# Kernel optimization log

Measured on AMD Instinct MI355X. Metric: run time of the kernel, lower is better.

The kernel has to match this reference:

```python
import jax, jax.numpy as jnp
import numpy as np

N_SRC0, N_FTRS, N_HID, N_CLS = 200000, 128, 1500, 64
E0, E1 = 1600000, 500000
RES0, RES1 = 50000, 10000


def sage_conv(x, src, tgt, res_size, W_root, W_neigh, b):
    # mean aggregation of neighbor (source) features onto the first res_size target nodes
    msg = x[src]                                              # [E, F] gather
    summed = jax.ops.segment_sum(msg, tgt, num_segments=res_size)   # [res, F]
    cnt = jax.ops.segment_sum(jnp.ones((src.shape[0],), x.dtype), tgt, num_segments=res_size)
    mean = summed / jnp.maximum(cnt, 1.0)[:, None]
    return x[:res_size] @ W_root + mean @ W_neigh + b


def setup_inputs() -> dict:
    key = jax.random.key(0)
    ks = jax.random.split(key, 12)
    x = jax.random.normal(ks[0], (N_SRC0, N_FTRS), dtype=jnp.float32)
    edge_src0 = jax.random.randint(ks[1], (E0,), 0, N_SRC0)
    edge_tgt0 = jax.random.randint(ks[2], (E0,), 0, RES0)
    edge_src1 = jax.random.randint(ks[3], (E1,), 0, RES0)
    edge_tgt1 = jax.random.randint(ks[4], (E1,), 0, RES1)
    s1 = 1.0 / np.sqrt(N_FTRS)
    s2 = 1.0 / np.sqrt(N_HID)
    W1_root = jax.random.uniform(ks[5], (N_FTRS, N_HID), jnp.float32, -s1, s1)
    W1_neigh = jax.random.uniform(ks[6], (N_FTRS, N_HID), jnp.float32, -s1, s1)
    b1 = jax.random.uniform(ks[7], (N_HID,), jnp.float32, -s1, s1)
    W2_root = jax.random.uniform(ks[8], (N_HID, N_CLS), jnp.float32, -s2, s2)
    W2_neigh = jax.random.uniform(ks[9], (N_HID, N_CLS), jnp.float32, -s2, s2)
    b2 = jax.random.uniform(ks[10], (N_CLS,), jnp.float32, -s2, s2)
    return {
        "x": x,
        "W1_root": W1_root, "W1_neigh": W1_neigh, "b1": b1,
        "W2_root": W2_root, "W2_neigh": W2_neigh, "b2": b2,
        "edge_src0": edge_src0, "edge_tgt0": edge_tgt0,
        "edge_src1": edge_src1, "edge_tgt1": edge_tgt1,
        "res0": RES0, "res1": RES1,
    }


def reference(x, W1_root, W1_neigh, b1, W2_root, W2_neigh, b2,
              edge_src0, edge_tgt0, edge_src1, edge_tgt1, res0, res1):
    h = sage_conv(x, edge_src0, edge_tgt0, res0, W1_root, W1_neigh, b1)  # [res0, H]
    h = jax.nn.relu(h)
    # dropout p=0.5 is identity in eval mode
    out = sage_conv(h, edge_src1, edge_tgt1, res1, W2_root, W2_neigh, b2)  # [res1, C]
    return jax.nn.log_softmax(out, axis=1)
```

## Files before the change

### kernel.cpp

```cpp
#include <hip/hip_runtime.h>
#include <hip/hip_bf16.h>
#include <cstdint>
#include <cstddef>

#define NSRC   200000
#define NF     128
#define NHID   1500
#define NHIDP  1536
#define NCLS   64
#define E0N    1600000
#define E1N    500000
#define RES0   50000
#define RES1   10000

#define CH     4096
#define NCH0   ((E0N + CH - 1) / CH)
#define NCH1   ((E1N + CH - 1) / CH)
#define NB0    ((RES0 + 255) / 256)
#define NB1    ((RES1 + 255) / 256)

#define PREP_BLOCKS  ((256 * NHIDP + 128 * NHIDP + NHIDP + 255) / 256)
#define COPYX_BLOCKS ((NSRC * NF) / (256 * 8))

typedef __bf16 bf16x8 __attribute__((ext_vector_type(8)));
typedef float  f32x4  __attribute__((ext_vector_type(4)));
typedef unsigned short u16x8 __attribute__((ext_vector_type(8)));
typedef unsigned int u32;
typedef unsigned long long u64;

__device__ __forceinline__ unsigned short f2bf(float f) {
    union { float f; unsigned u; } v; v.f = f;
    unsigned r = v.u + 0x7fffu + ((v.u >> 16) & 1u);
    return (unsigned short)(r >> 16);
}
__device__ __forceinline__ float bf2f(unsigned short b) {
    union { u32 u; float f; } v; v.u = ((u32)b) << 16;
    return v.f;
}

__device__ __forceinline__ void lds_dma16(const void* g, void* lds) {
    __builtin_amdgcn_global_load_lds(
        (const __attribute__((address_space(1))) unsigned int*)g,
        (__attribute__((address_space(3))) unsigned int*)lds, 16, 0, 0);
}

__device__ __forceinline__ void raw_barrier() {
    __asm__ volatile("s_barrier" ::: "memory");
}
__device__ __forceinline__ void wait_vm4() {
    __asm__ volatile("s_waitcnt vmcnt(4)" ::: "memory");
}
__device__ __forceinline__ void wait_vm0() {
    __asm__ volatile("s_waitcnt vmcnt(0)" ::: "memory");
}
__device__ __forceinline__ void wait_lgkm0() {
    __asm__ volatile("s_waitcnt lgkmcnt(0)" ::: "memory");
}

__global__ __launch_bounds__(256) void setup_kernel(
        const float* __restrict__ x, unsigned short* __restrict__ xbf,
        const float* __restrict__ W1r, const float* __restrict__ W1n,
        const float* __restrict__ b1,
        const float* __restrict__ W2r, const float* __restrict__ W2n,
        unsigned short* __restrict__ WcatT, unsigned short* __restrict__ W2catT,
        float* __restrict__ b1e) {
    int bid = blockIdx.x;
    if (bid < PREP_BLOCKS) {
        int id = bid * 256 + threadIdx.x;
        if (id < 256 * NHIDP) {
            int n = id >> 8, k = id & 255;
            float v = 0.f;
            if (n < NHID) v = (k < NF) ? W1r[k * NHID + n] : W1n[(k - NF) * NHID + n];
            WcatT[n * 256 + k] = f2bf(v);
        } else {
            int id2 = id - 256 * NHIDP;
            if (id2 < 128 * NHIDP) {
                int n = id2 / NHIDP, k = id2 % NHIDP;
                float v = 0.f;
                if (k < NHID) v = (n < 64) ? W2n[k * 64 + n] : W2r[k * 64 + (n - 64)];
                W2catT[n * NHIDP + k] = f2bf(v);
            } else {
                int c = id2 - 128 * NHIDP;
                if (c < NHIDP) b1e[c] = (c < NHID) ? b1[c] : 0.f;
            }
        }
    } else {
        size_t i = ((size_t)(bid - PREP_BLOCKS) * 256 + threadIdx.x) * 8;
        const float4* s = (const float4*)(x + i);
        float4 a = s[0], b = s[1];
        u16x8 o;
        o[0] = f2bf(a.x); o[1] = f2bf(a.y); o[2] = f2bf(a.z); o[3] = f2bf(a.w);
        o[4] = f2bf(b.x); o[5] = f2bf(b.y); o[6] = f2bf(b.z); o[7] = f2bf(b.w);
        *(u16x8*)(xbf + i) = o;
    }
}

__device__ __forceinline__ void p1a_body(const int* __restrict__ tgt, int n,
                                         int nb, u32* __restrict__ H, int c) {
    __shared__ u32 lhist[256];
    int tid = threadIdx.x;
    lhist[tid] = 0;
    __syncthreads();
#pragma unroll
    for (int it = 0; it < CH / 256; ++it) {
        int i = c * CH + it * 256 + tid;
        if (i < n) atomicAdd(&lhist[((u32)tgt[i]) >> 8], 1u);
    }
    __syncthreads();
    if (tid < nb) H[c * nb + tid] = lhist[tid];
}

__global__ __launch_bounds__(256) void p1a_both_kernel(
        const int* __restrict__ t0, const int* __restrict__ t1,
        u32* __restrict__ H1, u32* __restrict__ H2) {
    int b = blockIdx.x;
    if (b < NCH0) p1a_body(t0, E0N, NB0, H1, b);
    else          p1a_body(t1, E1N, NB1, H2, b - NCH0);
}

__device__ __forceinline__ void bscan_body(const u32* __restrict__ H,
                                           int nch, int nb, int b,
                                           u32* __restrict__ base_rel,
                                           u32* __restrict__ Bsum) {
    __shared__ u32 part[512];
    int t = threadIdx.x;
    part[t] = (t < nch) ? H[t * nb + b] : 0u;
    __syncthreads();
    for (int d = 1; d < 512; d <<= 1) {
        u32 v = part[t];
        u32 add = (t >= d) ? part[t - d] : 0u;
        __syncthreads();
        part[t] = v + add;
        __syncthreads();
    }
    if (t < nch) base_rel[t * nb + b] = (t == 0) ? 0u : part[t - 1];
    if (t == 0) Bsum[b] = part[nch - 1];
}

__global__ __launch_bounds__(512) void bscan_both_kernel(
        const u32* __restrict__ H1, u32* __restrict__ base1, u32* __restrict__ Bsum1,
        const u32* __restrict__ H2, u32* __restrict__ base2, u32* __restrict__ Bsum2) {
    int b = blockIdx.x;
    if (b < NB0) bscan_body(H1, NCH0, NB0, b, base1, Bsum1);
    else         bscan_body(H2, NCH1, NB1, b - NB0, base2, Bsum2);
}

__global__ __launch_bounds__(256) void boff_kernel(const u32* __restrict__ Bsum1,
                                                   u32* __restrict__ boff1, int nb1,
                                                   const u32* __restrict__ Bsum2,
                                                   u32* __restrict__ boff2, int nb2) {
    const u32* B = blockIdx.x ? Bsum2 : Bsum1;
    u32* O = blockIdx.x ? boff2 : boff1;
    int nb = blockIdx.x ? nb2 : nb1;
    __shared__ u32 part[256];
    int t = threadIdx.x;
    part[t] = (t < nb) ? B[t] : 0u;
    __syncthreads();
    for (int d = 1; d < 256; d <<= 1) {
        u32 v = part[t];
        u32 add = (t >= d) ? part[t - d] : 0u;
        __syncthreads();
        part[t] = v + add;
        __syncthreads();
    }
    if (t < nb) O[t] = (t == 0) ? 0u : part[t - 1];
}

__device__ __forceinline__ void p1b_body(const int* __restrict__ src,
                                         const int* __restrict__ tgt, int n,
                                         int nb, const u32* __restrict__ base_rel,
                                         const u32* __restrict__ boff,
                                         u64* __restrict__ bucketed, int c) {
    __shared__ u32 lcur[256];
    __shared__ u32 lbase[256];
    int tid = threadIdx.x;
    lcur[tid] = 0;
    if (tid < nb) lbase[tid] = base_rel[c * nb + tid] + boff[tid];
    __syncthreads();
#pragma unroll
    for (int it = 0; it < CH / 256; ++it) {
        int i = c * CH + it * 256 + tid;
        if (i < n) {
            u32 t = (u32)tgt[i];
            u32 s = (u32)src[i];
            u32 b = t >> 8;
            u32 r = atomicAdd(&lcur[b], 1u);
            bucketed[lbase[b] + r] = ((u64)t << 32) | (u64)s;
        }
    }
}

__global__ __launch_bounds__(256) void p1b_both_kernel(
        const int* __restrict__ s0, const int* __restrict__ t0,
        const u32* __restrict__ base1, const u32* __restrict__ boff1,
        u64* __restrict__ bkt1,
        const int* __restrict__ s1, const int* __restrict__ t1,
        const u32* __restrict__ base2, const u32* __restrict__ boff2,
        u64* __restrict__ bkt2) {
    int b = blockIdx.x;
    if (b < NCH0) p1b_body(s0, t0, E0N, NB0, base1, boff1, bkt1, b);
    else          p1b_body(s1, t1, E1N, NB1, base2, boff2, bkt2, b - NCH0);
}

__device__ __forceinline__ void p2_body(const u64* __restrict__ bucketed,
                                        const u32* __restrict__ boff,
                                        int nb, int res, int etot,
                                        int* __restrict__ csr,
                                        u32* __restrict__ off_out,
                                        u32* __restrict__ cnt_out, int b) {
    __shared__ u32 lhist[256];
    __shared__ u32 part[256];
    __shared__ u32 cur[256];
    int tid = threadIdx.x;
    u32 start = boff[b];
    u32 end = (b == nb - 1) ? (u32)etot : boff[b + 1];
    u32 count = end - start;
    if (tid < 256) lhist[tid] = 0;
    __syncthreads();
    for (u32 i = tid; i < count; i += 1024) {
        u32 t = (u32)(bucketed[start + i] >> 32);
        atomicAdd(&lhist[t & 255u], 1u);
    }
    __syncthreads();
    if (tid < 256) part[tid] = lhist[tid];
    __syncthreads();
    for (int d = 1; d < 256; d <<= 1) {
        u32 v = (tid < 256) ? part[tid] : 0u;
        u32 add = (tid >= d && tid < 256) ? part[tid - d] : 0u;
        __syncthreads();
        if (tid < 256) part[tid] = v + add;
        __syncthreads();
    }
    if (tid < 256) {
        u32 excl = (tid == 0) ? 0u : part[tid - 1];
        cur[tid] = excl;
        int tg = (b << 8) + tid;
        if (tg < res) {
            off_out[tg] = start + excl;
            cnt_out[tg] = lhist[tid];
        }
    }
    __syncthreads();
    for (u32 i = tid; i < count; i += 1024) {
        u64 pr = bucketed[start + i];
        u32 lt = ((u32)(pr >> 32)) & 255u;
        u32 r = atomicAdd(&cur[lt], 1u);
        csr[start + r] = (int)(u32)pr;
    }
}

__global__ __launch_bounds__(1024) void p2_both_kernel(
        const u64* __restrict__ bkt1, const u32* __restrict__ boff1,
        int* __restrict__ csr1, u32* __restrict__ off1, u32* __restrict__ cnt1,
        const u64* __restrict__ bkt2, const u32* __restrict__ boff2,
        int* __restrict__ csr2, u32* __restrict__ off2, u32* __restrict__ cnt2) {
    int b = blockIdx.x;
    if (b < NB0) p2_body(bkt1, boff1, NB0, RES0, E0N, csr1, off1, cnt1, b);
    else         p2_body(bkt2, boff2, NB1, RES1, E1N, csr2, off2, cnt2, b - NB0);
}

__global__ __launch_bounds__(256) void agg1_csr_kernel(
        const unsigned short* __restrict__ xbf, const int* __restrict__ csr,
        const u32* __restrict__ off, const u32* __restrict__ cnt,
        unsigned short* __restrict__ mean1) {
    int row = blockIdx.x * 4 + (threadIdx.x >> 6);
    int lane = threadIdx.x & 63;
    if (row >= RES0) return;
    int q = lane >> 4, c16 = lane & 15;
    u32 base = off[row], deg = cnt[row];
    float acc[8] = {};
    u32 e = 0;
    for (; e + 8 <= deg; e += 8) {
        int s0 = csr[base + e + q];
        int s1 = csr[base + e + 4 + q];
        u16x8 v0 = *(const u16x8*)(xbf + (size_t)s0 * NF + c16 * 8);
        u16x8 v1 = *(const u16x8*)(xbf + (size_t)s1 * NF + c16 * 8);
#pragma unroll
        for (int i = 0; i < 8; ++i) acc[i] += bf2f(v0[i]) + bf2f(v1[i]);
    }
    for (; e + 4 <= deg; e += 4) {
        int s0 = csr[base + e + q];
        u16x8 v0 = *(const u16x8*)(xbf + (size_t)s0 * NF + c16 * 8);
#pragma unroll
        for (int i = 0; i < 8; ++i) acc[i] += bf2f(v0[i]);
    }
    if (e < deg) {
        bool valid = (e + q) < deg;
        int s0 = csr[base + (valid ? e + q : e)];
        u16x8 v0 = *(const u16x8*)(xbf + (size_t)s0 * NF + c16 * 8);
        if (valid) {
#pragma unroll
            for (int i = 0; i < 8; ++i) acc[i] += bf2f(v0[i]);
        }
    }
#pragma unroll
    for (int i = 0; i < 8; ++i) {
        acc[i] += __shfl_xor(acc[i], 32, 64);
        acc[i] += __shfl_xor(acc[i], 16, 64);
    }
    if (q == 0) {
        float inv = 1.0f / fmaxf((float)deg, 1.0f);
        u16x8 o;
#pragma unroll
        for (int i = 0; i < 8; ++i) o[i] = f2bf(acc[i] * inv);
        *(u16x8*)(mean1 + (size_t)row * NF + c16 * 8) = o;
    }
}

__device__ __forceinline__ void stage_chunk(
        const unsigned short* __restrict__ xbf, const unsigned short* __restrict__ mean1,
        const unsigned short* __restrict__ WcatT, int m0, int j, int kt,
        unsigned short* As, unsigned short* Bs, int wid, int lane) {
    int ksel = kt * 32;
    const unsigned short* srcA = (ksel < 128)
        ? xbf + (size_t)m0 * NF + ksel
        : mean1 + (size_t)m0 * NF + (ksel - 128);
#pragma unroll
    for (int ci = 0; ci < 2; ++ci) {
        int cb = ci * 256 + wid * 64;
        int chunk = cb + lane;
        int n = chunk >> 2, kc = chunk & 3;
        lds_dma16(srcA + (size_t)n * NF + kc * 8, &As[cb * 8]);
    }
    const unsigned short* srcB = WcatT + (size_t)(j * 128) * 256 + ksel;
#pragma unroll
    for (int ci = 0; ci < 2; ++ci) {
        int cb = ci * 256 + wid * 64;
        int chunk = cb + lane;
        int n = chunk >> 2, kc = chunk & 3;
        lds_dma16(srcB + (size_t)n * 256 + kc * 8, &Bs[cb * 8]);
    }
}

__global__ __launch_bounds__(256, 2) void fused_gemm_kernel(
        const unsigned short* __restrict__ xbf, const unsigned short* __restrict__ mean1,
        const unsigned short* __restrict__ WcatT, const float* __restrict__ b1e,
        const unsigned short* __restrict__ W2catT,
        float* __restrict__ pp0, float* __restrict__ pp1) {
    __shared__ __align__(16) unsigned short As[3][128 * 32];
    __shared__ __align__(16) unsigned short Bs[3][128 * 32];
    __shared__ __align__(16) unsigned short Ht[128 * 128];

    int m0 = blockIdx.x * 128;
    int jb = blockIdx.y * 6;
    float* pout = blockIdx.y ? pp1 : pp0;
    int tid = threadIdx.x;
    int lane = tid & 63, wid = tid >> 6;
    int wm = wid >> 1, wn = wid & 1;
    int quad = lane >> 4, l15 = lane & 15;

    f32x4 pacc[4][4] = {};

    stage_chunk(xbf, mean1, WcatT, m0, jb, 0, As[0], Bs[0], wid, lane);
    stage_chunk(xbf, mean1, WcatT, m0, jb, 1, As[1], Bs[1], wid, lane);

#pragma unroll
    for (int jj = 0; jj < 6; ++jj) {
        int j = jb + jj;
        f32x4 hacc[4][4] = {};
#pragma unroll
        for (int kt = 0; kt < 8; ++kt) {
            const int g = jj * 8 + kt;
            if (g == 47) wait_vm0(); else wait_vm4();
            raw_barrier();
            if (g + 2 < 48) {
                int g2 = g + 2;
                stage_chunk(xbf, mean1, WcatT, m0, jb + (g2 >> 3), g2 & 7,
                            As[g2 % 3], Bs[g2 % 3], wid, lane);
            }
            const unsigned short* Asb = As[g % 3];
            const unsigned short* Bsb = Bs[g % 3];
            bf16x8 a[4], b[4];
#pragma unroll
            for (int mi = 0; mi < 4; ++mi)
                a[mi] = *(const bf16x8*)(&Asb[(wm * 64 + mi * 16 + l15) * 32 + quad * 8]);
#pragma unroll
            for (int ni = 0; ni < 4; ++ni)
                b[ni] = *(const bf16x8*)(&Bsb[(wn * 64 + ni * 16 + l15) * 32 + quad * 8]);
#pragma unroll
            for (int mi = 0; mi < 4; ++mi)
#pragma unroll
                for (int ni = 0; ni < 4; ++ni)
                    hacc[mi][ni] = __builtin_amdgcn_mfma_f32_16x16x32_bf16(b[ni], a[mi], hacc[mi][ni], 0, 0, 0);
        }
#pragma unroll
        for (int ni = 0; ni < 4; ++ni) {
            int n0 = wn * 64 + ni * 16 + quad * 4;
            float4 bv = *(const float4*)(b1e + j * 128 + n0);
#pragma unroll
            for (int mi = 0; mi < 4; ++mi) {
                int m = wm * 64 + mi * 16 + l15;
                int gsw = ((n0 >> 3) ^ (m & 15));
                ushort4 o;
                o.x = f2bf(fmaxf(hacc[mi][ni][0] + bv.x, 0.f));
                o.y = f2bf(fmaxf(hacc[mi][ni][1] + bv.y, 0.f));
                o.z = f2bf(fmaxf(hacc[mi][ni][2] + bv.z, 0.f));
                o.w = f2bf(fmaxf(hacc[mi][ni][3] + bv.w, 0.f));
                *(ushort4*)(&Ht[m * 128 + gsw * 8 + (n0 & 7)]) = o;
            }
        }
        wait_lgkm0();
        raw_barrier();
#pragma unroll
        for (int kk2 = 0; kk2 < 128; kk2 += 32) {
            bf16x8 a2[4], b2[4];
#pragma unroll
            for (int mi = 0; mi < 4; ++mi) {
                int m = wm * 64 + mi * 16 + l15;
                int gr = (kk2 >> 3) + quad;
                int gsw = gr ^ (m & 15);
                a2[mi] = *(const bf16x8*)(&Ht[m * 128 + gsw * 8]);
            }
#pragma unroll
            for (int ni = 0; ni < 4; ++ni)
                b2[ni] = *(const bf16x8*)(W2catT + (size_t)(wn * 64 + ni * 16 + l15) * NHIDP
                                          + j * 128 + kk2 + quad * 8);
#pragma unroll
            for (int mi = 0; mi < 4; ++mi)
#pragma unroll
                for (int ni = 0; ni < 4; ++ni)
                    pacc[mi][ni] = __builtin_amdgcn_mfma_f32_16x16x32_bf16(b2[ni], a2[mi], pacc[mi][ni], 0, 0, 0);
        }
    }

#pragma unroll
    for (int mi = 0; mi < 4; ++mi) {
        int gr = m0 + wm * 64 + mi * 16 + l15;
        if (gr < RES0) {
#pragma unroll
            for (int ni = 0; ni < 4; ++ni) {
                int gc0 = wn * 64 + ni * 16 + quad * 4;
                *(float4*)(&pout[(size_t)gr * 128 + gc0]) = *(float4*)(&pacc[mi][ni]);
            }
        }
    }
}

__global__ __launch_bounds__(256) void padd_kernel(
        const float* __restrict__ pp0, const float* __restrict__ pp1,
        unsigned short* __restrict__ pnbf, float* __restrict__ root64) {
    int i = blockIdx.x * 256 + threadIdx.x;
    if (i >= RES0 * 8) return;
    int row = i >> 3, c8 = i & 7;
    size_t b = (size_t)row * 128 + c8 * 8;
    f32x4 s0 = *(const f32x4*)(pp0 + b)     + *(const f32x4*)(pp1 + b);
    f32x4 s1 = *(const f32x4*)(pp0 + b + 4) + *(const f32x4*)(pp1 + b + 4);
    u16x8 o;
    o[0] = f2bf(s0[0]); o[1] = f2bf(s0[1]); o[2] = f2bf(s0[2]); o[3] = f2bf(s0[3]);
    o[4] = f2bf(s1[0]); o[5] = f2bf(s1[1]); o[6] = f2bf(s1[2]); o[7] = f2bf(s1[3]);
    *(u16x8*)(pnbf + (size_t)row * 64 + c8 * 8) = o;
    if (row < RES1) {
        size_t rb = (size_t)row * 128 + 64 + c8 * 8;
        f32x4 r0 = *(const f32x4*)(pp0 + rb)     + *(const f32x4*)(pp1 + rb);
        f32x4 r1 = *(const f32x4*)(pp0 + rb + 4) + *(const f32x4*)(pp1 + rb + 4);
        *(f32x4*)(root64 + (size_t)row * 64 + c8 * 8)     = r0;
        *(f32x4*)(root64 + (size_t)row * 64 + c8 * 8 + 4) = r1;
    }
}

__global__ __launch_bounds__(256) void final_csr_kernel(
        const unsigned short* __restrict__ pnbf, const float* __restrict__ root64,
        const int* __restrict__ csr, const u32* __restrict__ off,
        const u32* __restrict__ cnt, const float* __restrict__ b2,
        float* __restrict__ out) {
    int row = blockIdx.x * 4 + (threadIdx.x >> 6);
    int lane = threadIdx.x & 63;
    if (row >= RES1) return;
    int es = lane >> 3, c8 = lane & 7;
    u32 base = off[row], deg = cnt[row];
    float acc[8] = {};
    u32 e = 0;
    for (; e + 8 <= deg; e += 8) {
        int s = csr[base + e + es];
        u16x8 v = *(const u16x8*)(pnbf + (size_t)s * 64 + c8 * 8);
#pragma unroll
        for (int i = 0; i < 8; ++i) acc[i] += bf2f(v[i]);
    }
    if (e < deg) {
        bool valid = (e + es) < deg;
        int s = csr[base + (valid ? e + es : e)];
        u16x8 v = *(const u16x8*)(pnbf + (size_t)s * 64 + c8 * 8);
        if (valid) {
#pragma unroll
            for (int i = 0; i < 8; ++i) acc[i] += bf2f(v[i]);
        }
    }
#pragma unroll
    for (int i = 0; i < 8; ++i) {
        acc[i] += __shfl_xor(acc[i], 32, 64);
        acc[i] += __shfl_xor(acc[i], 16, 64);
        acc[i] += __shfl_xor(acc[i], 8, 64);
    }
    float inv = 1.0f / fmaxf((float)deg, 1.0f);
    float v[8];
    const float* rp = root64 + (size_t)row * 64 + c8 * 8;
#pragma unroll
    for (int i = 0; i < 8; ++i) v[i] = rp[i] + acc[i] * inv + b2[c8 * 8 + i];
    float m = v[0];
#pragma unroll
    for (int i = 1; i < 8; ++i) m = fmaxf(m, v[i]);
    m = fmaxf(m, __shfl_xor(m, 1, 64));
    m = fmaxf(m, __shfl_xor(m, 2, 64));
    m = fmaxf(m, __shfl_xor(m, 4, 64));
    float s = 0.f;
#pragma unroll
    for (int i = 0; i < 8; ++i) s += expf(v[i] - m);
    s += __shfl_xor(s, 1, 64);
    s += __shfl_xor(s, 2, 64);
    s += __shfl_xor(s, 4, 64);
    if (es == 0) {
        float lg = logf(s);
        f32x4 o0, o1;
#pragma unroll
        for (int i = 0; i < 4; ++i) { o0[i] = v[i] - m - lg; o1[i] = v[i + 4] - m - lg; }
        *(f32x4*)(&out[(size_t)row * 64 + c8 * 8])     = o0;
        *(f32x4*)(&out[(size_t)row * 64 + c8 * 8 + 4]) = o1;
    }
}

extern "C" void kernel_launch(void* const* d_in, const int* in_sizes, int n_in,
                              void* d_out, int out_size, void* d_ws, size_t ws_size,
                              hipStream_t stream) {
    const float* x   = (const float*)d_in[0];
    const float* W1r = (const float*)d_in[1];
    const float* W1n = (const float*)d_in[2];
    const float* b1  = (const float*)d_in[3];
    const float* W2r = (const float*)d_in[4];
    const float* W2n = (const float*)d_in[5];
    const float* b2  = (const float*)d_in[6];
    const int* es0 = (const int*)d_in[7];
    const int* et0 = (const int*)d_in[8];
    const int* es1 = (const int*)d_in[9];
    const int* et1 = (const int*)d_in[10];
    float* out = (float*)d_out;

    char* ws = (char*)d_ws;
    const size_t PPBYTES = (size_t)RES0 * 128 * 4;
    float* pp1 = (float*)ws;
    size_t o0 = 0;
    auto alloc0 = [&](size_t bytes) {
        void* ptr = ws + o0;
        o0 = (o0 + bytes + 255) & ~(size_t)255;
        return ptr;
    };
    u64* bkt1  = (u64*)alloc0((size_t)E0N * 8);
    u64* bkt2  = (u64*)alloc0((size_t)E1N * 8);
    int* csr1  = (int*)alloc0((size_t)E0N * 4);
    u32* H1    = (u32*)alloc0((size_t)NCH0 * NB0 * 4);
    u32* base1 = (u32*)alloc0((size_t)NCH0 * NB0 * 4);
    u32* H2    = (u32*)alloc0((size_t)NCH1 * NB1 * 4);
    u32* base2 = (u32*)alloc0((size_t)NCH1 * NB1 * 4);
    u32* Bsum1 = (u32*)alloc0((size_t)NB0 * 4);
    u32* Bsum2 = (u32*)alloc0((size_t)NB1 * 4);
    u32* boff1 = (u32*)alloc0((size_t)NB0 * 4);
    u32* boff2 = (u32*)alloc0((size_t)NB1 * 4);
    u32* off1  = (u32*)alloc0((size_t)RES0 * 4);
    u32* cnt1  = (u32*)alloc0((size_t)RES0 * 4);

    size_t off_ = PPBYTES;
    auto alloc = [&](size_t bytes) {
        void* ptr = ws + off_;
        off_ = (off_ + bytes + 255) & ~(size_t)255;
        return ptr;
    };
    int* csr2  = (int*)alloc((size_t)E1N * 4);
    u32* off2  = (u32*)alloc((size_t)RES1 * 4);
    u32* cnt2  = (u32*)alloc((size_t)RES1 * 4);
    unsigned short* xbf    = (unsigned short*)alloc((size_t)NSRC * NF * 2);
    unsigned short* mean1  = (unsigned short*)alloc((size_t)(RES0 + 128) * NF * 2);
    unsigned short* WcatT  = (unsigned short*)alloc((size_t)NHIDP * 256 * 2);
    unsigned short* W2catT = (unsigned short*)alloc((size_t)128 * NHIDP * 2);
    float*          b1e    = (float*)alloc((size_t)NHIDP * 4);
    float*          pp0    = (float*)alloc(PPBYTES);
    unsigned short* pnbf   = (unsigned short*)alloc((size_t)RES0 * 64 * 2);
    float*          root64 = (float*)alloc((size_t)RES1 * 64 * 4);

    setup_kernel<<<PREP_BLOCKS + COPYX_BLOCKS, 256, 0, stream>>>(
        x, xbf, W1r, W1n, b1, W2r, W2n, WcatT, W2catT, b1e);

    p1a_both_kernel<<<NCH0 + NCH1, 256, 0, stream>>>(et0, et1, H1, H2);
    bscan_both_kernel<<<NB0 + NB1, 512, 0, stream>>>(H1, base1, Bsum1, H2, base2, Bsum2);
    boff_kernel<<<2, 256, 0, stream>>>(Bsum1, boff1, NB0, Bsum2, boff2, NB1);
    p1b_both_kernel<<<NCH0 + NCH1, 256, 0, stream>>>(
        es0, et0, base1, boff1, bkt1, es1, et1, base2, boff2, bkt2);
    p2_both_kernel<<<NB0 + NB1, 1024, 0, stream>>>(
        bkt1, boff1, csr1, off1, cnt1, bkt2, boff2, csr2, off2, cnt2);

    agg1_csr_kernel<<<(RES0 + 3) / 4, 256, 0, stream>>>(
        xbf, csr1, off1, cnt1, mean1);

    fused_gemm_kernel<<<dim3((RES0 + 127) / 128, 2), 256, 0, stream>>>(
        xbf, mean1, WcatT, b1e, W2catT, pp0, pp1);

    padd_kernel<<<(RES0 * 8 + 255) / 256, 256, 0, stream>>>(pp0, pp1, pnbf, root64);

    final_csr_kernel<<<(RES1 + 3) / 4, 256, 0, stream>>>(
        pnbf, root64, csr2, off2, cnt2, b2, out);
}
```

Measured before the change: 444.2 us.

## Shrink fused GEMM tile to 64 rows and keep hidden activations in registers

```diff
diff --git a/kernel.cpp b/kernel.cpp
--- a/kernel.cpp
+++ b/kernel.cpp
@@ -38,6 +38,12 @@
     return v.f;
 }
 
+__device__ __forceinline__ u32 cvt_pk_bf16(float lo, float hi) {
+    u32 r;
+    asm("v_cvt_pk_bf16_f32 %0, %1, %2" : "=v"(r) : "v"(lo), "v"(hi));
+    return r;
+}
+
 __device__ __forceinline__ void lds_dma16(const void* g, void* lds) {
     __builtin_amdgcn_global_load_lds(
         (const __attribute__((address_space(1))) unsigned int*)g,
@@ -47,14 +53,11 @@
 __device__ __forceinline__ void raw_barrier() {
     __asm__ volatile("s_barrier" ::: "memory");
 }
-__device__ __forceinline__ void wait_vm4() {
-    __asm__ volatile("s_waitcnt vmcnt(4)" ::: "memory");
+__device__ __forceinline__ void wait_vm3() {
+    __asm__ volatile("s_waitcnt vmcnt(3)" ::: "memory");
 }
 __device__ __forceinline__ void wait_vm0() {
     __asm__ volatile("s_waitcnt vmcnt(0)" ::: "memory");
-}
-__device__ __forceinline__ void wait_lgkm0() {
-    __asm__ volatile("s_waitcnt lgkmcnt(0)" ::: "memory");
 }
 
 __global__ __launch_bounds__(256) void setup_kernel(
@@ -307,41 +310,14 @@
     }
 }
 
-__device__ __forceinline__ void stage_chunk(
-        const unsigned short* __restrict__ xbf, const unsigned short* __restrict__ mean1,
-        const unsigned short* __restrict__ WcatT, int m0, int j, int kt,
-        unsigned short* As, unsigned short* Bs, int wid, int lane) {
-    int ksel = kt * 32;
-    const unsigned short* srcA = (ksel < 128)
-        ? xbf + (size_t)m0 * NF + ksel
-        : mean1 + (size_t)m0 * NF + (ksel - 128);
-#pragma unroll
-    for (int ci = 0; ci < 2; ++ci) {
-        int cb = ci * 256 + wid * 64;
-        int chunk = cb + lane;
-        int n = chunk >> 2, kc = chunk & 3;
-        lds_dma16(srcA + (size_t)n * NF + kc * 8, &As[cb * 8]);
-    }
-    const unsigned short* srcB = WcatT + (size_t)(j * 128) * 256 + ksel;
-#pragma unroll
-    for (int ci = 0; ci < 2; ++ci) {
-        int cb = ci * 256 + wid * 64;
-        int chunk = cb + lane;
-        int n = chunk >> 2, kc = chunk & 3;
-        lds_dma16(srcB + (size_t)n * 256 + kc * 8, &Bs[cb * 8]);
-    }
-}
-
-__global__ __launch_bounds__(256, 2) void fused_gemm_kernel(
+__global__ __launch_bounds__(256, 3) void fused_gemm_kernel(
         const unsigned short* __restrict__ xbf, const unsigned short* __restrict__ mean1,
         const unsigned short* __restrict__ WcatT, const float* __restrict__ b1e,
         const unsigned short* __restrict__ W2catT,
         float* __restrict__ pp0, float* __restrict__ pp1) {
-    __shared__ __align__(16) unsigned short As[3][128 * 32];
-    __shared__ __align__(16) unsigned short Bs[3][128 * 32];
-    __shared__ __align__(16) unsigned short Ht[128 * 128];
-
-    int m0 = blockIdx.x * 128;
+    __shared__ __align__(16) unsigned short buf[3][6144];
+
+    int m0 = blockIdx.x * 64;
     int jb = blockIdx.y * 6;
     float* pout = blockIdx.y ? pp1 : pp0;
     int tid = threadIdx.x;
@@ -349,90 +325,117 @@
     int wm = wid >> 1, wn = wid & 1;
     int quad = lane >> 4, l15 = lane & 15;
 
-    f32x4 pacc[4][4] = {};
-
-    stage_chunk(xbf, mean1, WcatT, m0, jb, 0, As[0], Bs[0], wid, lane);
-    stage_chunk(xbf, mean1, WcatT, m0, jb, 1, As[1], Bs[1], wid, lane);
+    const int rA = lane >> 2, kcs = (lane & 3) * 8;
+    const size_t offA = (size_t)rA * NF + kcs;
+    const size_t offB = (size_t)rA * 256 + kcs;
+    const unsigned short* Ax = xbf + (size_t)m0 * NF;
+    const unsigned short* Am = mean1 + (size_t)m0 * NF;
+
+    auto stage = [&](int g) {
+        int ksel = (g & 7) * 32;
+        const unsigned short* Asrc = (ksel < 128) ? (Ax + ksel) : (Am + (ksel - 128));
+        const unsigned short* Bsrc = WcatT + ((size_t)(jb + (g >> 3)) * 128) * 256 + ksel;
+        unsigned short* dst = &buf[g % 3][0];
+#pragma unroll
+        for (int i = 0; i < 3; ++i) {
+            int id = wid * 3 + i;
+            if (id < 4) lds_dma16(Asrc + (size_t)id * (16 * NF) + offA, dst + id * 512);
+            else        lds_dma16(Bsrc + (size_t)(id - 4) * (16 * 256) + offB, dst + id * 512);
+        }
+    };
+
+    f32x4 pacc[2][8] = {};
+
+    stage(0);
+    stage(1);
 
 #pragma unroll
     for (int jj = 0; jj < 6; ++jj) {
-        int j = jb + jj;
-        f32x4 hacc[4][4] = {};
+        const int j = jb + jj;
+        f32x4 hacc[2][4] = {};
 #pragma unroll
         for (int kt = 0; kt < 8; ++kt) {
             const int g = jj * 8 + kt;
-            if (g == 47) wait_vm0(); else wait_vm4();
+            if (g == 47) wait_vm0(); else wait_vm3();
             raw_barrier();
-            if (g + 2 < 48) {
-                int g2 = g + 2;
-                stage_chunk(xbf, mean1, WcatT, m0, jb + (g2 >> 3), g2 & 7,
-                            As[g2 % 3], Bs[g2 % 3], wid, lane);
-            }
-            const unsigned short* Asb = As[g % 3];
-            const unsigned short* Bsb = Bs[g % 3];
-            bf16x8 a[4], b[4];
-#pragma unroll
-            for (int mi = 0; mi < 4; ++mi)
-                a[mi] = *(const bf16x8*)(&Asb[(wm * 64 + mi * 16 + l15) * 32 + quad * 8]);
+            if (g + 2 < 48) stage(g + 2);
+            const unsigned short* Ab = &buf[g % 3][0];
+            const unsigned short* Bb = Ab + 2048;
+            bf16x8 a[2], b[4];
+#pragma unroll
+            for (int mi = 0; mi < 2; ++mi)
+                a[mi] = *(const bf16x8*)(Ab + (wm * 32 + mi * 16 + l15) * 32 + quad * 8);
 #pragma unroll
             for (int ni = 0; ni < 4; ++ni)
-                b[ni] = *(const bf16x8*)(&Bsb[(wn * 64 + ni * 16 + l15) * 32 + quad * 8]);
-#pragma unroll
-            for (int mi = 0; mi < 4; ++mi)
+                b[ni] = *(const bf16x8*)(Bb + (wn * 64 + ni * 16 + l15) * 32 + quad * 8);
+            __builtin_amdgcn_s_setprio(1);
+#pragma unroll
+            for (int mi = 0; mi < 2; ++mi)
 #pragma unroll
                 for (int ni = 0; ni < 4; ++ni)
                     hacc[mi][ni] = __builtin_amdgcn_mfma_f32_16x16x32_bf16(b[ni], a[mi], hacc[mi][ni], 0, 0, 0);
-        }
-#pragma unroll
-        for (int ni = 0; ni < 4; ++ni) {
-            int n0 = wn * 64 + ni * 16 + quad * 4;
-            float4 bv = *(const float4*)(b1e + j * 128 + n0);
-#pragma unroll
-            for (int mi = 0; mi < 4; ++mi) {
-                int m = wm * 64 + mi * 16 + l15;
-                int gsw = ((n0 >> 3) ^ (m & 15));
-                ushort4 o;
-                o.x = f2bf(fmaxf(hacc[mi][ni][0] + bv.x, 0.f));
-                o.y = f2bf(fmaxf(hacc[mi][ni][1] + bv.y, 0.f));
-                o.z = f2bf(fmaxf(hacc[mi][ni][2] + bv.z, 0.f));
-                o.w = f2bf(fmaxf(hacc[mi][ni][3] + bv.w, 0.f));
-                *(ushort4*)(&Ht[m * 128 + gsw * 8 + (n0 & 7)]) = o;
+            __builtin_amdgcn_s_setprio(0);
+        }
+
+        u32 a2w[2][2][4];
+#pragma unroll
+        for (int mi = 0; mi < 2; ++mi)
+#pragma unroll
+            for (int ni = 0; ni < 4; ++ni) {
+                float4 bv = *(const float4*)(b1e + j * 128 + wn * 64 + ni * 16 + quad * 4);
+                f32x4 h = hacc[mi][ni];
+                float h0 = fmaxf(h[0] + bv.x, 0.f);
+                float h1 = fmaxf(h[1] + bv.y, 0.f);
+                float h2 = fmaxf(h[2] + bv.z, 0.f);
+                float h3 = fmaxf(h[3] + bv.w, 0.f);
+                a2w[mi][ni >> 1][(ni & 1) * 2 + 0] = cvt_pk_bf16(h0, h1);
+                a2w[mi][ni >> 1][(ni & 1) * 2 + 1] = cvt_pk_bf16(h2, h3);
             }
-        }
-        wait_lgkm0();
-        raw_barrier();
-#pragma unroll
-        for (int kk2 = 0; kk2 < 128; kk2 += 32) {
-            bf16x8 a2[4], b2[4];
-#pragma unroll
-            for (int mi = 0; mi < 4; ++mi) {
-                int m = wm * 64 + mi * 16 + l15;
-                int gr = (kk2 >> 3) + quad;
-                int gsw = gr ^ (m & 15);
-                a2[mi] = *(const bf16x8*)(&Ht[m * 128 + gsw * 8]);
+        const unsigned short* W2p = W2catT + (size_t)(j * 128 + wn * 64 + quad * 4);
+        __builtin_amdgcn_s_setprio(1);
+#pragma unroll
+        for (int kk = 0; kk < 2; ++kk) {
+            union U { u32 w[4]; bf16x8 v; };
+            U A2[2];
+#pragma unroll
+            for (int mi = 0; mi < 2; ++mi)
+#pragma unroll
+                for (int w = 0; w < 4; ++w) A2[mi].w[w] = a2w[mi][kk][w];
+#pragma unroll
+            for (int ni2 = 0; ni2 < 8; ++ni2) {
+                size_t bb = (size_t)(ni2 * 16 + l15) * NHIDP + kk * 32;
+                uint2 lo = *(const uint2*)(W2p + bb);
+                uint2 hi = *(const uint2*)(W2p + bb + 16);
+                U B2; B2.w[0] = lo.x; B2.w[1] = lo.y; B2.w[2] = hi.x; B2.w[3] = hi.y;
+#pragma unroll
+                for (int mi = 0; mi < 2; ++mi)
+                    pacc[mi][ni2] = __builtin_amdgcn_mfma_f32_16x16x32_bf16(B2.v, A2[mi].v, pacc[mi][ni2], 0, 0, 0);
             }
-#pragma unroll
-            for (int ni = 0; ni < 4; ++ni)
-                b2[ni] = *(const bf16x8*)(W2catT + (size_t)(wn * 64 + ni * 16 + l15) * NHIDP
-                                          + j * 128 + kk2 + quad * 8);
-#pragma unroll
-            for (int mi = 0; mi < 4; ++mi)
-#pragma unroll
-                for (int ni = 0; ni < 4; ++ni)
-                    pacc[mi][ni] = __builtin_amdgcn_mfma_f32_16x16x32_bf16(b2[ni], a2[mi], pacc[mi][ni], 0, 0, 0);
-        }
-    }
-
-#pragma unroll
-    for (int mi = 0; mi < 4; ++mi) {
-        int gr = m0 + wm * 64 + mi * 16 + l15;
-        if (gr < RES0) {
-#pragma unroll
-            for (int ni = 0; ni < 4; ++ni) {
-                int gc0 = wn * 64 + ni * 16 + quad * 4;
-                *(float4*)(&pout[(size_t)gr * 128 + gc0]) = *(float4*)(&pacc[mi][ni]);
+        }
+        __builtin_amdgcn_s_setprio(0);
+    }
+
+    __syncthreads();
+    float* red = (float*)&buf[0][0];
+#pragma unroll
+    for (int mi = 0; mi < 2; ++mi) {
+        if (wn == 1) {
+#pragma unroll
+            for (int ni2 = 0; ni2 < 8; ++ni2)
+                *(f32x4*)(red + wm * 2048 + ni2 * 256 + lane * 4) = pacc[mi][ni2];
+        }
+        __syncthreads();
+        if (wn == 0) {
+            int gr = m0 + wm * 32 + mi * 16 + l15;
+            if (gr < RES0) {
+#pragma unroll
+                for (int ni2 = 0; ni2 < 8; ++ni2) {
+                    f32x4 s = pacc[mi][ni2] + *(const f32x4*)(red + wm * 2048 + ni2 * 256 + lane * 4);
+                    *(f32x4*)(&pout[(size_t)gr * 128 + ni2 * 16 + quad * 4]) = s;
+                }
             }
         }
+        __syncthreads();
     }
 }
 
@@ -589,7 +592,7 @@
     agg1_csr_kernel<<<(RES0 + 3) / 4, 256, 0, stream>>>(
         xbf, csr1, off1, cnt1, mean1);
 
-    fused_gemm_kernel<<<dim3((RES0 + 127) / 128, 2), 256, 0, stream>>>(
+    fused_gemm_kernel<<<dim3((RES0 + 63) / 64, 2), 256, 0, stream>>>(
         xbf, mean1, WcatT, b1e, W2catT, pp0, pp1);
 
     padd_kernel<<<(RES0 * 8 + 255) / 256, 256, 0, stream>>>(pp0, pp1, pnbf, root64);
```

Result: slower. 652.5 us (+46.9%).

## Drop split-K over hidden dim in fused GEMM, removing partial-sum reduction kernel

Applied to the files above, without the earlier changes.

```diff
diff --git a/kernel.cpp b/kernel.cpp
--- a/kernel.cpp
+++ b/kernel.cpp
@@ -336,14 +336,12 @@
         const unsigned short* __restrict__ xbf, const unsigned short* __restrict__ mean1,
         const unsigned short* __restrict__ WcatT, const float* __restrict__ b1e,
         const unsigned short* __restrict__ W2catT,
-        float* __restrict__ pp0, float* __restrict__ pp1) {
+        unsigned short* __restrict__ pnbf, float* __restrict__ root64) {
     __shared__ __align__(16) unsigned short As[3][128 * 32];
     __shared__ __align__(16) unsigned short Bs[3][128 * 32];
     __shared__ __align__(16) unsigned short Ht[128 * 128];
 
     int m0 = blockIdx.x * 128;
-    int jb = blockIdx.y * 6;
-    float* pout = blockIdx.y ? pp1 : pp0;
     int tid = threadIdx.x;
     int lane = tid & 63, wid = tid >> 6;
     int wm = wid >> 1, wn = wid & 1;
@@ -351,21 +349,21 @@
 
     f32x4 pacc[4][4] = {};
 
-    stage_chunk(xbf, mean1, WcatT, m0, jb, 0, As[0], Bs[0], wid, lane);
-    stage_chunk(xbf, mean1, WcatT, m0, jb, 1, As[1], Bs[1], wid, lane);
-
-#pragma unroll
-    for (int jj = 0; jj < 6; ++jj) {
-        int j = jb + jj;
+    stage_chunk(xbf, mean1, WcatT, m0, 0, 0, As[0], Bs[0], wid, lane);
+    stage_chunk(xbf, mean1, WcatT, m0, 0, 1, As[1], Bs[1], wid, lane);
+
+#pragma unroll 1
+    for (int jj = 0; jj < 12; ++jj) {
+        const int j = jj;
         f32x4 hacc[4][4] = {};
 #pragma unroll
         for (int kt = 0; kt < 8; ++kt) {
             const int g = jj * 8 + kt;
-            if (g == 47) wait_vm0(); else wait_vm4();
+            if (g == 95) wait_vm0(); else wait_vm4();
             raw_barrier();
-            if (g + 2 < 48) {
+            if (g + 2 < 96) {
                 int g2 = g + 2;
-                stage_chunk(xbf, mean1, WcatT, m0, jb + (g2 >> 3), g2 & 7,
+                stage_chunk(xbf, mean1, WcatT, m0, g2 >> 3, g2 & 7,
                             As[g2 % 3], Bs[g2 % 3], wid, lane);
             }
             const unsigned short* Asb = As[g % 3];
@@ -429,32 +427,18 @@
         if (gr < RES0) {
 #pragma unroll
             for (int ni = 0; ni < 4; ++ni) {
-                int gc0 = wn * 64 + ni * 16 + quad * 4;
-                *(float4*)(&pout[(size_t)gr * 128 + gc0]) = *(float4*)(&pacc[mi][ni]);
+                f32x4 s = pacc[mi][ni];
+                int c0 = ni * 16 + quad * 4;
+                if (wn == 0) {
+                    uint2 o;
+                    o.x = (u32)f2bf(s[0]) | ((u32)f2bf(s[1]) << 16);
+                    o.y = (u32)f2bf(s[2]) | ((u32)f2bf(s[3]) << 16);
+                    *(uint2*)(pnbf + (size_t)gr * 64 + c0) = o;
+                } else if (gr < RES1) {
+                    *(f32x4*)(root64 + (size_t)gr * 64 + c0) = s;
+                }
             }
         }
-    }
-}
-
-__global__ __launch_bounds__(256) void padd_kernel(
-        const float* __restrict__ pp0, const float* __restrict__ pp1,
-        unsigned short* __restrict__ pnbf, float* __restrict__ root64) {
-    int i = blockIdx.x * 256 + threadIdx.x;
-    if (i >= RES0 * 8) return;
-    int row = i >> 3, c8 = i & 7;
-    size_t b = (size_t)row * 128 + c8 * 8;
-    f32x4 s0 = *(const f32x4*)(pp0 + b)     + *(const f32x4*)(pp1 + b);
-    f32x4 s1 = *(const f32x4*)(pp0 + b + 4) + *(const f32x4*)(pp1 + b + 4);
-    u16x8 o;
-    o[0] = f2bf(s0[0]); o[1] = f2bf(s0[1]); o[2] = f2bf(s0[2]); o[3] = f2bf(s0[3]);
-    o[4] = f2bf(s1[0]); o[5] = f2bf(s1[1]); o[6] = f2bf(s1[2]); o[7] = f2bf(s1[3]);
-    *(u16x8*)(pnbf + (size_t)row * 64 + c8 * 8) = o;
-    if (row < RES1) {
-        size_t rb = (size_t)row * 128 + 64 + c8 * 8;
-        f32x4 r0 = *(const f32x4*)(pp0 + rb)     + *(const f32x4*)(pp1 + rb);
-        f32x4 r1 = *(const f32x4*)(pp0 + rb + 4) + *(const f32x4*)(pp1 + rb + 4);
-        *(f32x4*)(root64 + (size_t)row * 64 + c8 * 8)     = r0;
-        *(f32x4*)(root64 + (size_t)row * 64 + c8 * 8 + 4) = r1;
     }
 }
 
@@ -535,34 +519,25 @@
     float* out = (float*)d_out;
 
     char* ws = (char*)d_ws;
-    const size_t PPBYTES = (size_t)RES0 * 128 * 4;
-    float* pp1 = (float*)ws;
-    size_t o0 = 0;
-    auto alloc0 = [&](size_t bytes) {
-        void* ptr = ws + o0;
-        o0 = (o0 + bytes + 255) & ~(size_t)255;
-        return ptr;
-    };
-    u64* bkt1  = (u64*)alloc0((size_t)E0N * 8);
-    u64* bkt2  = (u64*)alloc0((size_t)E1N * 8);
-    int* csr1  = (int*)alloc0((size_t)E0N * 4);
-    u32* H1    = (u32*)alloc0((size_t)NCH0 * NB0 * 4);
-    u32* base1 = (u32*)alloc0((size_t)NCH0 * NB0 * 4);
-    u32* H2    = (u32*)alloc0((size_t)NCH1 * NB1 * 4);
-    u32* base2 = (u32*)alloc0((size_t)NCH1 * NB1 * 4);
-    u32* Bsum1 = (u32*)alloc0((size_t)NB0 * 4);
-    u32* Bsum2 = (u32*)alloc0((size_t)NB1 * 4);
-    u32* boff1 = (u32*)alloc0((size_t)NB0 * 4);
-    u32* boff2 = (u32*)alloc0((size_t)NB1 * 4);
-    u32* off1  = (u32*)alloc0((size_t)RES0 * 4);
-    u32* cnt1  = (u32*)alloc0((size_t)RES0 * 4);
-
-    size_t off_ = PPBYTES;
+    size_t off_ = 0;
     auto alloc = [&](size_t bytes) {
         void* ptr = ws + off_;
         off_ = (off_ + bytes + 255) & ~(size_t)255;
         return ptr;
     };
+    u64* bkt1  = (u64*)alloc((size_t)E0N * 8);
+    u64* bkt2  = (u64*)alloc((size_t)E1N * 8);
+    int* csr1  = (int*)alloc((size_t)E0N * 4);
+    u32* H1    = (u32*)alloc((size_t)NCH0 * NB0 * 4);
+    u32* base1 = (u32*)alloc((size_t)NCH0 * NB0 * 4);
+    u32* H2    = (u32*)alloc((size_t)NCH1 * NB1 * 4);
+    u32* base2 = (u32*)alloc((size_t)NCH1 * NB1 * 4);
+    u32* Bsum1 = (u32*)alloc((size_t)NB0 * 4);
+    u32* Bsum2 = (u32*)alloc((size_t)NB1 * 4);
+    u32* boff1 = (u32*)alloc((size_t)NB0 * 4);
+    u32* boff2 = (u32*)alloc((size_t)NB1 * 4);
+    u32* off1  = (u32*)alloc((size_t)RES0 * 4);
+    u32* cnt1  = (u32*)alloc((size_t)RES0 * 4);
     int* csr2  = (int*)alloc((size_t)E1N * 4);
     u32* off2  = (u32*)alloc((size_t)RES1 * 4);
     u32* cnt2  = (u32*)alloc((size_t)RES1 * 4);
@@ -571,7 +546,6 @@
     unsigned short* WcatT  = (unsigned short*)alloc((size_t)NHIDP * 256 * 2);
     unsigned short* W2catT = (unsigned short*)alloc((size_t)128 * NHIDP * 2);
     float*          b1e    = (float*)alloc((size_t)NHIDP * 4);
-    float*          pp0    = (float*)alloc(PPBYTES);
     unsigned short* pnbf   = (unsigned short*)alloc((size_t)RES0 * 64 * 2);
     float*          root64 = (float*)alloc((size_t)RES1 * 64 * 4);
 
@@ -589,10 +563,8 @@
     agg1_csr_kernel<<<(RES0 + 3) / 4, 256, 0, stream>>>(
         xbf, csr1, off1, cnt1, mean1);
 
-    fused_gemm_kernel<<<dim3((RES0 + 127) / 128, 2), 256, 0, stream>>>(
-        xbf, mean1, WcatT, b1e, W2catT, pp0, pp1);
-
-    padd_kernel<<<(RES0 * 8 + 255) / 256, 256, 0, stream>>>(pp0, pp1, pnbf, root64);
+    fused_gemm_kernel<<<(RES0 + 127) / 128, 256, 0, stream>>>(
+        xbf, mean1, WcatT, b1e, W2catT, pnbf, root64);
 
     final_csr_kernel<<<(RES1 + 3) / 4, 256, 0, stream>>>(
         pnbf, root64, csr2, off2, cnt2, b2, out);
```

Result: faster. 435.5 us (-2.0%).
